# Kernel tuning notes

Measured on AMD Instinct MI355X. Metric: run time of the kernel, lower is better.

## Reference

```python
import jax, jax.numpy as jnp
import numpy as np

MARGIN = 0.35
SCALE = 64.0
EPS = 1e-8  # torch F.cosine_similarity norm clamp


def setup_inputs() -> dict:
    key = jax.random.key(0)
    k1, k2 = jax.random.split(key)
    N, D = 8192, 512
    embeddings = jax.random.normal(k1, (N, D), dtype=jnp.float32)
    labels = jax.random.randint(k2, (N,), 0, 128, dtype=jnp.int64)
    return {"embeddings": embeddings, "labels": labels}


def reference(embeddings, labels):
    # cosine similarity as Gram matrix of norm-clamped-normalized rows
    norms = jnp.maximum(jnp.linalg.norm(embeddings, axis=1, keepdims=True), EPS)
    e = embeddings / norms                      # [N, D]
    sim = jnp.einsum('id,jd->ij', e, e)         # [N, N]
    pos_mask = (labels[:, None] == labels[None, :]).astype(sim.dtype)
    # pos_sim - neg_sim = sim*mask - sim*(1-mask) = sim*(2*mask - 1)
    signed = sim * (2.0 * pos_mask - 1.0)
    loss = jnp.log1p(jnp.exp(-SCALE * (signed - MARGIN)))
    return jnp.mean(loss)
```

## Files before the change

kernel.cpp:

```cpp
#include <hip/hip_runtime.h>


typedef unsigned short u16;
typedef unsigned int u32;
typedef __attribute__((ext_vector_type(4))) float f32x4;
typedef __attribute__((ext_vector_type(8))) short bf16x8;
typedef __attribute__((ext_vector_type(8))) u16 u16x8;

#define AS1 __attribute__((address_space(1)))
#define AS3 __attribute__((address_space(3)))

__global__ __launch_bounds__(256) void norm_bf16_k(
    const float* __restrict__ emb, u16* __restrict__ e, int N, int D) {
  const int wid = threadIdx.x >> 6, lane = threadIdx.x & 63;
  const int row = blockIdx.x * 4 + wid;
  if (row >= N) return;
  const float* p = emb + (size_t)row * D + lane * 8;
  f32x4 a = *(const f32x4*)p;
  f32x4 b = *(const f32x4*)(p + 4);
  float ss = 0.f;
#pragma unroll
  for (int i = 0; i < 4; ++i) ss += a[i] * a[i] + b[i] * b[i];
#pragma unroll
  for (int o = 32; o >= 1; o >>= 1) ss += __shfl_xor(ss, o, 64);
  const float inv = 1.0f / fmaxf(sqrtf(ss), 1e-8f);
  u16x8 hv;
#pragma unroll
  for (int i = 0; i < 8; ++i) {
    float x = (i < 4 ? a[i] : b[i - 4]) * inv;
    u32 u = __float_as_uint(x);
    u += 0x7FFFu + ((u >> 16) & 1u);
    hv[i] = (u16)(u >> 16);
  }
  *(u16x8*)(e + (size_t)row * D + lane * 8) = hv;
}

__global__ __launch_bounds__(512, 2) void gram_loss_k(
    const u16* __restrict__ e, const int* __restrict__ labels,
    float* __restrict__ out, int N, int D, int NT, int nwg, float invNN) {
  __shared__ __attribute__((aligned(16))) u16 sL[2][2][32 * 512];
  __shared__ float swred[8];

  const int tid = threadIdx.x, wid = tid >> 6, lane = tid & 63;

  const int q8 = nwg >> 3, r8 = nwg & 7;
  const int x = blockIdx.x & 7, p = blockIdx.x >> 3;
  const int bid = (x < r8 ? x * (q8 + 1) : r8 * (q8 + 1) + (x - r8) * q8) + p;

  int I = 0, rem = bid, rl = NT;
  while (rem >= rl) { rem -= rl; ++I; --rl; }
  const int J = I + rem;
  const int i0 = I * 256, j0 = J * 256;

  const int ab = wid >> 2;
  const int rbase = ab ? j0 : i0;
  const int f0 = (wid & 3) * 8;
  u32 goff[8];
#pragma unroll
  for (int q = 0; q < 8; ++q) {
    const int f = f0 + q, mf = f >> 1, ks = f & 1;
    goff[q] = (u32)(rbase + mf * 16 + (lane & 15)) * (u32)D + ks * 32 +
              ((lane >> 4) * 8);
  }

  const f32x4 z = {0.f, 0.f, 0.f, 0.f};
  f32x4 acc[8][4];
#pragma unroll
  for (int m = 0; m < 8; ++m)
#pragma unroll
    for (int n = 0; n < 4; ++n) acc[m][n] = z;

  const int wr = wid >> 2, wc = wid & 3;

  auto stage = [&](int buf, int kk) {
#pragma unroll
    for (int q = 0; q < 8; ++q)
      __builtin_amdgcn_global_load_lds((const AS1 void*)(e + goff[q] + kk),
                                       (AS3 void*)(&sL[buf][ab][(f0 + q) * 512]),
                                       16, 0, 0);
  };

  stage(0, 0);

#pragma unroll
  for (int t = 0; t < 8; ++t) {
    const int buf = t & 1;
    asm volatile("s_waitcnt vmcnt(0)" ::: "memory");
    __builtin_amdgcn_s_barrier();
    if (t < 7) stage(buf ^ 1, (t + 1) * 64);
#pragma unroll
    for (int ks = 0; ks < 2; ++ks) {
      bf16x8 b[4];
#pragma unroll
      for (int n = 0; n < 4; ++n)
        b[n] = *(const bf16x8*)&sL[buf][1][(((wc * 4 + n) << 1) + ks) * 512 + lane * 8];
#pragma unroll
      for (int mh = 0; mh < 2; ++mh) {
        bf16x8 a[4];
#pragma unroll
        for (int m = 0; m < 4; ++m)
          a[m] = *(const bf16x8*)&sL[buf][0]
                     [(((wr * 8 + mh * 4 + m) << 1) + ks) * 512 + lane * 8];
        __builtin_amdgcn_s_setprio(1);
#pragma unroll
        for (int m = 0; m < 4; ++m)
#pragma unroll
          for (int n = 0; n < 4; ++n)
            acc[mh * 4 + m][n] = __builtin_amdgcn_mfma_f32_16x16x32_bf16(
                a[m], b[n], acc[mh * 4 + m][n], 0, 0, 0);
        __builtin_amdgcn_s_setprio(0);
      }
    }
  }

  const float C0 = 64.0f * 0.35f;
  float lsum = 0.f;
  const int rb = i0 + wr * 128, cb = j0 + wc * 64;
#pragma unroll
  for (int m = 0; m < 8; ++m) {
    const int gi0 = rb + m * 16 + (lane >> 4) * 4;
#pragma unroll
    for (int n = 0; n < 4; ++n) {
      const int gj = cb + n * 16 + (lane & 15);
      const int lj = labels[gj];
#pragma unroll
      for (int r = 0; r < 4; ++r) {
        const int li = labels[gi0 + r];
        float s = acc[m][n][r];
        float sg = (li == lj) ? s : -s;
        float xv = fmaf(-64.0f, sg, C0);
        float ax = fabsf(xv);
        lsum += fmaxf(xv, 0.f) + __logf(1.0f + __expf(-ax));
      }
    }
  }

#pragma unroll
  for (int o = 32; o >= 1; o >>= 1) lsum += __shfl_xor(lsum, o, 64);
  if (lane == 0) swred[wid] = lsum;
  __syncthreads();
  if (tid == 0) {
    float t = 0.f;
#pragma unroll
    for (int w = 0; w < 8; ++w) t += swred[w];
    const float wgt = (I == J) ? 1.0f : 2.0f;
    atomicAdd(out, t * wgt * invNN);
  }
}

extern "C" void kernel_launch(void* const* d_in, const int* in_sizes, int n_in,
                              void* d_out, int out_size, void* d_ws, size_t ws_size,
                              hipStream_t stream) {
  const float* emb = (const float*)d_in[0];
  const int* labels = (const int*)d_in[1];
  float* out = (float*)d_out;

  const int N = in_sizes[1];
  const int D = in_sizes[0] / N;
  const int NT = N / 256;
  const int nTiles = NT * (NT + 1) / 2;

  u16* e = (u16*)d_ws;

  hipMemsetAsync(out, 0, sizeof(float), stream);
  norm_bf16_k<<<N / 4, 256, 0, stream>>>(emb, e, N, D);
  gram_loss_k<<<nTiles, 512, 0, stream>>>(e, labels, out, N, D, NT, nTiles,
                                          (float)(1.0 / ((double)N * (double)N)));
}
```

Baseline: 164.1 us.

## Software-pipeline Gram tile loads into fine-grained phases and cache labels in LDS

Replaces the two-stage per-K-step loop with a hand-scheduled pipeline. The A and B operand fragments are now loaded in quarter-sized chunks interleaved between MFMA phases, with partial vmcnt waits and barriers, so global-to-LDS transfers overlap compute more finely. The epilogue reads labels from a shared-memory copy of the tile's 512 labels instead of issuing global loads per element. The cost is more barriers per iteration and a tricky buffer-reuse schedule that is fragile if the wait counts are wrong.

```diff
diff --git a/kernel.cpp b/kernel.cpp
--- a/kernel.cpp
+++ b/kernel.cpp
@@ -39,29 +39,24 @@
     const u16* __restrict__ e, const int* __restrict__ labels,
     float* __restrict__ out, int N, int D, int NT, int nwg, float invNN) {
   __shared__ __attribute__((aligned(16))) u16 sL[2][2][32 * 512];
+  __shared__ int sLab[512];
   __shared__ float swred[8];
 
   const int tid = threadIdx.x, wid = tid >> 6, lane = tid & 63;
 
   const int q8 = nwg >> 3, r8 = nwg & 7;
-  const int x = blockIdx.x & 7, p = blockIdx.x >> 3;
-  const int bid = (x < r8 ? x * (q8 + 1) : r8 * (q8 + 1) + (x - r8) * q8) + p;
+  const int xx = blockIdx.x & 7, pp = blockIdx.x >> 3;
+  const int bid = (xx < r8 ? xx * (q8 + 1) : r8 * (q8 + 1) + (xx - r8) * q8) + pp;
 
   int I = 0, rem = bid, rl = NT;
   while (rem >= rl) { rem -= rl; ++I; --rl; }
   const int J = I + rem;
   const int i0 = I * 256, j0 = J * 256;
 
-  const int ab = wid >> 2;
-  const int rbase = ab ? j0 : i0;
-  const int f0 = (wid & 3) * 8;
-  u32 goff[8];
-#pragma unroll
-  for (int q = 0; q < 8; ++q) {
-    const int f = f0 + q, mf = f >> 1, ks = f & 1;
-    goff[q] = (u32)(rbase + mf * 16 + (lane & 15)) * (u32)D + ks * 32 +
-              ((lane >> 4) * 8);
-  }
+  if (tid < 256) sLab[tid] = labels[i0 + tid];
+  else           sLab[tid] = labels[j0 + tid - 256];
+
+  const int wr = wid >> 2, wc = wid & 3;
 
   const f32x4 z = {0.f, 0.f, 0.f, 0.f};
   f32x4 acc[8][4];
@@ -70,62 +65,96 @@
 #pragma unroll
     for (int n = 0; n < 4; ++n) acc[m][n] = z;
 
-  const int wr = wid >> 2, wc = wid & 3;
+  bf16x8 b[4][2];
 
-  auto stage = [&](int buf, int kk) {
-#pragma unroll
-    for (int q = 0; q < 8; ++q)
-      __builtin_amdgcn_global_load_lds((const AS1 void*)(e + goff[q] + kk),
-                                       (AS3 void*)(&sL[buf][ab][(f0 + q) * 512]),
-                                       16, 0, 0);
-  };
+#define STG(BUF, OP, TILE, H)                                                 \
+  {                                                                           \
+    _Pragma("unroll") for (int j = 0; j < 2; ++j) {                           \
+      const int frag = (H) * 16 + wid + 8 * j;                                \
+      const u32 off = (u32)(((OP) ? j0 : i0) + (frag >> 1) * 16 + (lane & 15)) \
+                          * (u32)D +                                          \
+                      (TILE) * 64 + (frag & 1) * 32 + ((lane >> 4) * 8);      \
+      __builtin_amdgcn_global_load_lds((const AS1 void*)(e + off),            \
+                                       (AS3 void*)(&sL[BUF][OP][frag * 512]), \
+                                       16, 0, 0);                             \
+    }                                                                         \
+  }
 
-  stage(0, 0);
+#define RD_B(BUF)                                                             \
+  _Pragma("unroll") for (int n = 0; n < 4; ++n)                               \
+  _Pragma("unroll") for (int ks = 0; ks < 2; ++ks)                            \
+      b[n][ks] = *(const bf16x8*)&sL[BUF][1]                                  \
+                     [(((wc * 4 + n) << 1) + ks) * 512 + lane * 8];
 
-#pragma unroll
-  for (int t = 0; t < 8; ++t) {
-    const int buf = t & 1;
-    asm volatile("s_waitcnt vmcnt(0)" ::: "memory");
-    __builtin_amdgcn_s_barrier();
-    if (t < 7) stage(buf ^ 1, (t + 1) * 64);
-#pragma unroll
-    for (int ks = 0; ks < 2; ++ks) {
-      bf16x8 b[4];
-#pragma unroll
-      for (int n = 0; n < 4; ++n)
-        b[n] = *(const bf16x8*)&sL[buf][1][(((wc * 4 + n) << 1) + ks) * 512 + lane * 8];
-#pragma unroll
-      for (int mh = 0; mh < 2; ++mh) {
-        bf16x8 a[4];
-#pragma unroll
-        for (int m = 0; m < 4; ++m)
-          a[m] = *(const bf16x8*)&sL[buf][0]
-                     [(((wr * 8 + mh * 4 + m) << 1) + ks) * 512 + lane * 8];
-        __builtin_amdgcn_s_setprio(1);
-#pragma unroll
-        for (int m = 0; m < 4; ++m)
-#pragma unroll
-          for (int n = 0; n < 4; ++n)
-            acc[mh * 4 + m][n] = __builtin_amdgcn_mfma_f32_16x16x32_bf16(
-                a[m], b[n], acc[mh * 4 + m][n], 0, 0, 0);
-        __builtin_amdgcn_s_setprio(0);
-      }
-    }
+#define VMCNT4 asm volatile("s_waitcnt vmcnt(4)" ::: "memory");
+#define VMCNT0 asm volatile("s_waitcnt vmcnt(0)" ::: "memory");
+
+#define PH(BUF, QP, STGS, WAITS)                                              \
+  {                                                                           \
+    bf16x8 a[2][2];                                                           \
+    _Pragma("unroll") for (int mm = 0; mm < 2; ++mm)                          \
+    _Pragma("unroll") for (int ks = 0; ks < 2; ++ks)                          \
+        a[mm][ks] = *(const bf16x8*)&sL[BUF][0]                               \
+            [(((wr * 8 + (QP) * 2 + mm) << 1) + ks) * 512 + lane * 8];        \
+    STGS;                                                                     \
+    WAITS;                                                                    \
+    __builtin_amdgcn_s_barrier();                                             \
+    asm volatile("s_waitcnt lgkmcnt(0)" ::: "memory");                        \
+    __builtin_amdgcn_sched_barrier(0);                                        \
+    __builtin_amdgcn_s_setprio(1);                                            \
+    _Pragma("unroll") for (int mm = 0; mm < 2; ++mm)                          \
+    _Pragma("unroll") for (int n = 0; n < 4; ++n)                             \
+    _Pragma("unroll") for (int ks = 0; ks < 2; ++ks)                          \
+        acc[(QP) * 2 + mm][n] = __builtin_amdgcn_mfma_f32_16x16x32_bf16(      \
+            a[mm][ks], b[n][ks], acc[(QP) * 2 + mm][n], 0, 0, 0);             \
+    __builtin_amdgcn_s_setprio(0);                                            \
+    __builtin_amdgcn_s_barrier();                                             \
   }
+
+#define ITER_STD(V, W, X)                                                     \
+  RD_B(0) PH(0, 0, STG(1, 0, V, 0), ;)                                        \
+  PH(0, 1, STG(1, 0, V, 1), ;)                                                \
+  PH(0, 2, STG(0, 1, W, 0), ;)                                                \
+  PH(0, 3, STG(0, 1, W, 1), VMCNT4)                                           \
+  RD_B(1) PH(1, 0, STG(0, 0, W, 0), ;)                                        \
+  PH(1, 1, STG(0, 0, W, 1), ;)                                                \
+  PH(1, 2, STG(1, 1, X, 0), ;)                                                \
+  PH(1, 3, STG(1, 1, X, 1), VMCNT4)
+
+  STG(0, 0, 0, 0) STG(0, 0, 0, 1) STG(0, 1, 0, 0) STG(0, 1, 0, 1)
+  STG(1, 1, 1, 0) STG(1, 1, 1, 1)
+  VMCNT4
+  __builtin_amdgcn_s_barrier();
+
+  ITER_STD(1, 2, 3)
+  ITER_STD(3, 4, 5)
+  ITER_STD(5, 6, 7)
+  RD_B(0) PH(0, 0, STG(1, 0, 7, 0), ;)
+  PH(0, 1, STG(1, 0, 7, 1), ;)
+  PH(0, 2, ;, ;)
+  PH(0, 3, ;, VMCNT0)
+  RD_B(1) PH(1, 0, ;, ;)
+  PH(1, 1, ;, ;)
+  PH(1, 2, ;, ;)
+  PH(1, 3, ;, ;)
+
+#undef ITER_STD
+#undef PH
+#undef RD_B
+#undef STG
 
   const float C0 = 64.0f * 0.35f;
   float lsum = 0.f;
-  const int rb = i0 + wr * 128, cb = j0 + wc * 64;
 #pragma unroll
   for (int m = 0; m < 8; ++m) {
-    const int gi0 = rb + m * 16 + (lane >> 4) * 4;
+    const int ri0 = wr * 128 + m * 16 + (lane >> 4) * 4;
 #pragma unroll
     for (int n = 0; n < 4; ++n) {
-      const int gj = cb + n * 16 + (lane & 15);
-      const int lj = labels[gj];
+      const int cj = wc * 64 + n * 16 + (lane & 15);
+      const int lj = sLab[256 + cj];
 #pragma unroll
       for (int r = 0; r < 4; ++r) {
-        const int li = labels[gi0 + r];
+        const int li = sLab[ri0 + r];
         float s = acc[m][n][r];
         float sg = (li == lj) ? s : -s;
         float xv = fmaf(-64.0f, sg, C0);
```

New measurement: 161.1 us. Within noise of the previous version (-1.8%).
